# Performance work log

Hardware: AMD Instinct MI355X
Metric: run time of the kernel (lower is better)

The kernel has to match this reference:

```python
import jax, jax.numpy as jnp
import numpy as np

LIDAR_MAX_X = 32.0
LIDAR_MAX_Y = 32.0


def bilinear_grid_sample(value, grid):
    """torch.nn.functional.grid_sample, mode='bilinear', padding_mode='zeros',
    align_corners=False.
    value: (B, C, H, W); grid: (B, Q, P, 2) in [-1, 1] (x=width, y=height).
    Returns (B, C, Q, P)."""
    B, C, H, W = value.shape
    x = (grid[..., 0] + 1.0) * (W / 2) - 0.5  # (B,Q,P) unnormalized col
    y = (grid[..., 1] + 1.0) * (H / 2) - 0.5  # (B,Q,P) unnormalized row
    x0 = jnp.floor(x)
    y0 = jnp.floor(y)
    x1 = x0 + 1.0
    y1 = y0 + 1.0
    wx1 = x - x0
    wx0 = 1.0 - wx1
    wy1 = y - y0
    wy0 = 1.0 - wy1
    vflat = value.reshape(B, C, H * W)

    def gather(ix, iy):
        valid = (ix >= 0) & (ix <= W - 1) & (iy >= 0) & (iy <= H - 1)
        ixc = jnp.clip(ix, 0, W - 1).astype(jnp.int32)
        iyc = jnp.clip(iy, 0, H - 1).astype(jnp.int32)
        idx = iyc * W + ixc  # (B,Q,P)
        g = jax.vmap(lambda v, i: v[:, i])(vflat, idx)  # (B,C,Q,P)
        return g * valid[:, None, :, :].astype(value.dtype)

    out = (gather(x0, y0) * (wx0 * wy0)[:, None]
           + gather(x1, y0) * (wx1 * wy0)[:, None]
           + gather(x0, y1) * (wx0 * wy1)[:, None]
           + gather(x1, y1) * (wx1 * wy1)[:, None])
    return out


def setup_inputs() -> dict:
    key = jax.random.key(0)
    ks = jax.random.split(key, 10)
    bs, Q, P, D = 16, 1024, 8, 256
    Cin, H, W = 64, 128, 128
    queries = jax.random.normal(ks[0], (bs, Q, D), dtype=jnp.float32)
    # scale so trajectory points span the +/-32m BEV extent
    traj_points = jax.random.normal(ks[1], (bs, Q, P, 2), dtype=jnp.float32) * 20.0
    bev_feature = jax.random.normal(ks[2], (bs, Cin, H, W), dtype=jnp.float32)
    spatial_shape = jnp.array([H, W], dtype=jnp.int64)
    attn_w = jax.random.normal(ks[3], (P, D), dtype=jnp.float32) * 0.02
    attn_b = jnp.zeros((P,), dtype=jnp.float32)
    conv_w = jax.random.normal(ks[4], (256, Cin, 3, 3), dtype=jnp.float32) * 0.05
    conv_b = jnp.zeros((256,), dtype=jnp.float32)
    out_w = jax.random.normal(ks[5], (D, D), dtype=jnp.float32) * (1.0 / np.sqrt(D))
    out_b = jnp.zeros((D,), dtype=jnp.float32)
    return {"queries": queries, "traj_points": traj_points,
            "bev_feature": bev_feature, "spatial_shape": spatial_shape,
            "attn_w": attn_w, "attn_b": attn_b,
            "conv_w": conv_w, "conv_b": conv_b,
            "out_w": out_w, "out_b": out_b}


def reference(queries, traj_points, bev_feature, spatial_shape,
              attn_w, attn_b, conv_w, conv_b, out_w, out_b):
    # normalize trajectory to [-1,1] and swap (y,x) -> (x,y) grid order
    grid = jnp.stack([traj_points[..., 1] / LIDAR_MAX_X,
                      traj_points[..., 0] / LIDAR_MAX_Y], axis=-1)  # (bs,Q,P,2)
    # per-query attention over the P sampled points
    attn = jax.nn.softmax(
        jnp.einsum('bqd,pd->bqp', queries, attn_w) + attn_b, axis=-1)  # (bs,Q,P)
    # value projection: 3x3 conv + ReLU
    value = jax.lax.conv_general_dilated(
        bev_feature, conv_w, window_strides=(1, 1),
        padding=((1, 1), (1, 1)),
        dimension_numbers=('NCHW', 'OIHW', 'NCHW'))
    value = jax.nn.relu(value + conv_b[None, :, None, None])  # (bs,256,H,W)
    sampled = bilinear_grid_sample(value, grid)  # (bs,256,Q,P)
    out = jnp.einsum('bcqp,bqp->bqc', sampled, attn)  # weighted sum + permute
    out = jnp.einsum('bqc,dc->bqd', out, out_w) + out_b
    # dropout is identity in eval mode
    return out + queries
```

## Files before the change

### kernel.cpp

```cpp
#include <hip/hip_runtime.h>
#include <stdint.h>


typedef __attribute__((ext_vector_type(8))) short short8;
typedef __attribute__((ext_vector_type(4))) float f32x4;

__device__ __forceinline__ unsigned short f2bf(float f) {
  union { float f; unsigned int u; } v; v.f = f;
  unsigned int r = (v.u + 0x7FFFu + ((v.u >> 16) & 1u)) >> 16;
  return (unsigned short)r;
}
__device__ __forceinline__ float bf2f(unsigned short h) {
  union { unsigned int u; float f; } v; v.u = ((unsigned int)h) << 16;
  return v.f;
}

__device__ __forceinline__ void gload_lds16(const void* g, void* l) {
  __builtin_amdgcn_global_load_lds(
      (const __attribute__((address_space(1))) unsigned int*)g,
      (__attribute__((address_space(3))) unsigned int*)l, 16, 0, 0);
}

__global__ __launch_bounds__(256) void k1_transpose(const float* __restrict__ bev,
                                                    unsigned short* __restrict__ nhwc) {
  __shared__ __align__(16) float lds[64 * 32 * 4];
  const int b = blockIdx.x >> 7, y = blockIdx.x & 127;
  const int t = threadIdx.x;
  const float* src = bev + (size_t)(b * 64) * 16384 + y * 128;
#pragma unroll
  for (int k = 0; k < 8; ++k) {
    int chunk = k * 256 + t;
    int ic = chunk >> 5, xq = chunk & 31;
    float4 v = *(const float4*)(src + ic * 16384 + xq * 4);
    int slot = xq ^ (ic >> 3);
    *(float4*)&lds[(ic * 32 + slot) * 4] = v;
  }
  __syncthreads();
  unsigned short* dst = nhwc + (size_t)blockIdx.x * 8192;
#pragma unroll
  for (int k = 0; k < 4; ++k) {
    int co = k * 256 + t;
    int x = co >> 3, icg = co & 7;
    int slot = (x >> 2) ^ icg;
    int w = x & 3;
    uint4 u;
    unsigned int* up = (unsigned int*)&u;
#pragma unroll
    for (int jj = 0; jj < 4; ++jj) {
      float v0 = lds[((icg * 8 + 2 * jj) * 32 + slot) * 4 + w];
      float v1 = lds[((icg * 8 + 2 * jj + 1) * 32 + slot) * 4 + w];
      up[jj] = (unsigned int)f2bf(v0) | ((unsigned int)f2bf(v1) << 16);
    }
    *(uint4*)(dst + x * 64 + icg * 8) = u;
  }
}

__global__ __launch_bounds__(256) void k1b_pack(const float* __restrict__ conv_w,
                                                const float* __restrict__ out_w,
                                                unsigned short* __restrict__ wconv,
                                                unsigned short* __restrict__ wout,
                                                float* __restrict__ zp) {
  const int tid = blockIdx.x * 256 + threadIdx.x;
  for (int idx = tid; idx < 9 * 8 * 256 * 8; idx += 16384) {
    int j = idx & 7, oc = (idx >> 3) & 255, g = (idx >> 11) & 7, o = idx >> 14;
    wconv[idx] = f2bf(conv_w[(oc * 64 + g * 8 + j) * 9 + o]);
  }
  for (int idx = tid; idx < 32 * 256 * 8; idx += 16384) {
    int j = idx & 7, d = (idx >> 3) & 255, g = idx >> 11;
    wout[idx] = f2bf(out_w[d * 256 + g * 8 + j]);
  }
  if (tid < 64) zp[tid] = 0.0f;
}

#define K2_LOADA(s, A) do {                                                   \
    _Pragma("unroll")                                                         \
    for (int ocf_ = 0; ocf_ < 8; ++ocf_)                                      \
      A[ocf_] = gA[(4 * (s) + g) * 256 + wo * 128 + ocf_ * 16 + l15];         \
  } while (0)

#define K2_READB(s, B) do {                                                   \
    const int o_ = (s) >> 1, ich_ = (s) & 1;                                  \
    const int dyr_ = o_ / 3, dx_ = o_ - dyr_ * 3 - 1;                         \
    _Pragma("unroll")                                                         \
    for (int pf_ = 0; pf_ < 4; ++pf_)                                         \
      B[pf_] = lin[((rh + dyr_) * 8 + ich_ * 4 + g) * 130 + 1 + dx_ + xb +    \
                   l15 + pf_ * 16];                                           \
  } while (0)

#define K2_MFMA(A, B) do {                                                    \
    __builtin_amdgcn_s_setprio(1);                                            \
    _Pragma("unroll")                                                         \
    for (int ocf_ = 0; ocf_ < 8; ++ocf_)                                      \
      _Pragma("unroll")                                                       \
      for (int pf_ = 0; pf_ < 4; ++pf_)                                       \
        acc[ocf_][pf_] = __builtin_amdgcn_mfma_f32_16x16x32_bf16(             \
            A[ocf_], B[pf_], acc[ocf_][pf_], 0, 0, 0);                        \
    __builtin_amdgcn_s_setprio(0);                                            \
  } while (0)

__global__ __launch_bounds__(512, 2) void k2_conv(const unsigned short* __restrict__ nhwc,
                                                  const unsigned short* __restrict__ wconv,
                                                  const float* __restrict__ conv_b,
                                                  const float* __restrict__ zp,
                                                  unsigned short* __restrict__ value) {
  __shared__ __align__(16) char smem[66560];
  const short8* lin = (const short8*)smem;
  const short8* gA = (const short8*)wconv;
  const int bid = blockIdx.x;
  const int swz = (bid & 7) * 128 + (bid >> 3);
  const int b = swz >> 6, yp = swz & 63;
  const int y0 = yp * 2;
  const int t = threadIdx.x, wid = t >> 6, lane = t & 63;
  const int wo = wid >> 2, wp = wid & 3;
  const int g = lane >> 4, l15 = lane & 15;
  const int rh = wp >> 1;
  const int xb = (wp & 1) * 64;

  const unsigned short* bevb = nhwc + (size_t)b * (128 * 128 * 64);
  for (int i = wid; i < 65; i += 8) {
    const int chunk = i * 64 + lane;
    const int ridx = chunk / 1040;
    const int rem = chunk - ridx * 1040;
    const int icg = rem / 130;
    const int c = rem - icg * 130;
    const int yy = y0 - 1 + ridx, xx = c - 1;
    const void* src = (yy >= 0 && yy < 128 && xx >= 0 && xx < 128)
                          ? (const void*)(bevb + ((yy * 128 + xx) * 64 + icg * 8))
                          : (const void*)zp;
    gload_lds16(src, smem + i * 1024);
  }
  __syncthreads();

  const f32x4 z4 = {0.f, 0.f, 0.f, 0.f};
  f32x4 acc[8][4];
#pragma unroll
  for (int i = 0; i < 8; ++i)
#pragma unroll
    for (int j = 0; j < 4; ++j) acc[i][j] = z4;

  short8 A[2][8], bb[2][4];
  K2_LOADA(0, A[0]);
  K2_LOADA(1, A[1]);
  K2_READB(0, bb[0]);

#pragma unroll
  for (int s = 0; s < 18; ++s) {
    if (s < 17) K2_READB(s + 1, bb[(s + 1) & 1]);
    K2_MFMA(A[s & 1], bb[s & 1]);
    if (s + 2 < 18) K2_LOADA(s + 2, A[s & 1]);
  }

  const int y = y0 + rh;
  unsigned short* vrow = value + (((size_t)(b * 128 + y) * 128 + xb + l15) * 256);
#pragma unroll
  for (int ocf = 0; ocf < 8; ++ocf) {
    const int ocb = wo * 128 + ocf * 16 + g * 4;
    const float4 cb4 = *(const float4*)(conv_b + ocb);
#pragma unroll
    for (int pf = 0; pf < 4; ++pf) {
      ushort4 ov;
      float v0 = acc[ocf][pf][0] + cb4.x; ov.x = f2bf(v0 > 0.f ? v0 : 0.f);
      float v1 = acc[ocf][pf][1] + cb4.y; ov.y = f2bf(v1 > 0.f ? v1 : 0.f);
      float v2 = acc[ocf][pf][2] + cb4.z; ov.z = f2bf(v2 > 0.f ? v2 : 0.f);
      float v3 = acc[ocf][pf][3] + cb4.w; ov.w = f2bf(v3 > 0.f ? v3 : 0.f);
      *(ushort4*)(vrow + (size_t)pf * 16 * 256 + ocb) = ov;
    }
  }
}

__global__ __launch_bounds__(256) void k3_sample(const float* __restrict__ queries,
                                                 const float* __restrict__ traj,
                                                 const float* __restrict__ attn_w,
                                                 const float* __restrict__ attn_b,
                                                 const unsigned short* __restrict__ value,
                                                 unsigned short* __restrict__ S) {
  const int wid = threadIdx.x >> 6, lane = threadIdx.x & 63;
  const int qg = blockIdx.x * 4 + wid;
  const int b = qg >> 10;
  const float4 qv = ((const float4*)queries)[qg * 64 + lane];
  float a[8];
#pragma unroll
  for (int p = 0; p < 8; ++p) {
    float4 wv = ((const float4*)attn_w)[p * 64 + lane];
    float d = qv.x * wv.x + qv.y * wv.y + qv.z * wv.z + qv.w * wv.w;
#pragma unroll
    for (int off = 32; off >= 1; off >>= 1) d += __shfl_xor(d, off);
    a[p] = d + attn_b[p];
  }
  float mx = a[0];
#pragma unroll
  for (int p = 1; p < 8; ++p) mx = fmaxf(mx, a[p]);
  float ssum = 0.f;
#pragma unroll
  for (int p = 0; p < 8; ++p) { a[p] = __expf(a[p] - mx); ssum += a[p]; }
  const float inv = 1.f / ssum;

  float acc0 = 0.f, acc1 = 0.f, acc2 = 0.f, acc3 = 0.f;
  const unsigned short* vb = value + (size_t)b * (128 * 128 * 256);
  const int coff = lane * 4;
#pragma unroll
  for (int p = 0; p < 8; ++p) {
    const float ty = traj[(qg * 8 + p) * 2 + 0];
    const float tx = traj[(qg * 8 + p) * 2 + 1];
    const float fx = (tx * 0.03125f + 1.f) * 64.f - 0.5f;
    const float fy = (ty * 0.03125f + 1.f) * 64.f - 0.5f;
    const float fx0 = floorf(fx), fy0 = floorf(fy);
    const int ix0 = (int)fx0, iy0 = (int)fy0;
    const float wx1 = fx - fx0, wx0 = 1.f - wx1;
    const float wy1 = fy - fy0, wy0 = 1.f - wy1;
    const float ap = a[p] * inv;
    const float cw[4] = {wx0 * wy0 * ap, wx1 * wy0 * ap, wx0 * wy1 * ap, wx1 * wy1 * ap};
    const int cx[4] = {ix0, ix0 + 1, ix0, ix0 + 1};
    const int cy[4] = {iy0, iy0, iy0 + 1, iy0 + 1};
#pragma unroll
    for (int cc = 0; cc < 4; ++cc) {
      if (cx[cc] >= 0 && cx[cc] < 128 && cy[cc] >= 0 && cy[cc] < 128) {
        const ushort4 v = *(const ushort4*)(vb + (cy[cc] * 128 + cx[cc]) * 256 + coff);
        acc0 += cw[cc] * bf2f(v.x);
        acc1 += cw[cc] * bf2f(v.y);
        acc2 += cw[cc] * bf2f(v.z);
        acc3 += cw[cc] * bf2f(v.w);
      }
    }
  }
  ushort4 o;
  o.x = f2bf(acc0); o.y = f2bf(acc1); o.z = f2bf(acc2); o.w = f2bf(acc3);
  *(ushort4*)(S + (size_t)qg * 256 + coff) = o;
}

__global__ __launch_bounds__(256, 2) void k4_proj(const unsigned short* __restrict__ S,
                                                  const unsigned short* __restrict__ wout,
                                                  const float* __restrict__ out_b,
                                                  const float* __restrict__ queries,
                                                  float* __restrict__ out) {
  __shared__ __align__(16) char smem[16384];
  const short8* lds8 = (const short8*)smem;
  const short8* wp8 = (const short8*)wout;
  const int t = threadIdx.x, wid = t >> 6, lane = t & 63;
  const int wo = wid >> 1, wq = wid & 1;
  const int q0 = blockIdx.x * 128;
  const int g = lane >> 4, l15 = lane & 15;
  const f32x4 z4 = {0.f, 0.f, 0.f, 0.f};
  f32x4 acc[8][4];
#pragma unroll
  for (int i = 0; i < 8; ++i)
#pragma unroll
    for (int j = 0; j < 4; ++j) acc[i][j] = z4;

#pragma unroll
  for (int ii = 0; ii < 2; ++ii) {
    const int chunk = wid * 128 + ii * 64 + lane;
    const int gg = chunk >> 7, q = chunk & 127;
    gload_lds16(S + ((size_t)(q0 + q) * 256 + gg * 8), smem + wid * 2048 + ii * 1024);
  }
  __syncthreads();

#pragma unroll
  for (int ks = 0; ks < 8; ++ks) {
    if (ks < 7) {
      const int k1 = ks + 1;
#pragma unroll
      for (int ii = 0; ii < 2; ++ii) {
        const int chunk = wid * 128 + ii * 64 + lane;
        const int gg = chunk >> 7, q = chunk & 127;
        gload_lds16(S + ((size_t)(q0 + q) * 256 + k1 * 32 + gg * 8),
                    smem + ((k1 & 1) ? 8192 : 0) + wid * 2048 + ii * 1024);
      }
    }
    short8 af[8];
#pragma unroll
    for (int df = 0; df < 8; ++df)
      af[df] = wp8[(ks * 4 + g) * 256 + wo * 128 + df * 16 + l15];
    short8 bf[4];
    const short8* sb = lds8 + ((ks & 1) ? 512 : 0);
#pragma unroll
    for (int qf = 0; qf < 4; ++qf) bf[qf] = sb[g * 128 + wq * 64 + qf * 16 + l15];
    __builtin_amdgcn_s_setprio(1);
#pragma unroll
    for (int df = 0; df < 8; ++df)
#pragma unroll
      for (int qf = 0; qf < 4; ++qf)
        acc[df][qf] = __builtin_amdgcn_mfma_f32_16x16x32_bf16(af[df], bf[qf], acc[df][qf], 0, 0, 0);
    __builtin_amdgcn_s_setprio(0);
    __syncthreads();
  }

#pragma unroll
  for (int df = 0; df < 8; ++df) {
    const int db = wo * 128 + df * 16 + g * 4;
    const float4 ob4 = *(const float4*)(out_b + db);
#pragma unroll
    for (int qf = 0; qf < 4; ++qf) {
      const int q = q0 + wq * 64 + qf * 16 + l15;
      const float4 qv = *(const float4*)(queries + (size_t)q * 256 + db);
      float4 ov;
      ov.x = acc[df][qf][0] + ob4.x + qv.x;
      ov.y = acc[df][qf][1] + ob4.y + qv.y;
      ov.z = acc[df][qf][2] + ob4.z + qv.z;
      ov.w = acc[df][qf][3] + ob4.w + qv.w;
      *(float4*)(out + (size_t)q * 256 + db) = ov;
    }
  }
}

extern "C" void kernel_launch(void* const* d_in, const int* in_sizes, int n_in,
                              void* d_out, int out_size, void* d_ws, size_t ws_size,
                              hipStream_t stream) {
  const float* queries = (const float*)d_in[0];
  const float* traj    = (const float*)d_in[1];
  const float* bev     = (const float*)d_in[2];
  const float* attn_w  = (const float*)d_in[4];
  const float* attn_b  = (const float*)d_in[5];
  const float* conv_w  = (const float*)d_in[6];
  const float* conv_b  = (const float*)d_in[7];
  const float* out_w   = (const float*)d_in[8];
  const float* out_b   = (const float*)d_in[9];
  float* out = (float*)d_out;

  char* ws = (char*)d_ws;
  unsigned short* bev_nhwc = (unsigned short*)(ws);
  unsigned short* value    = (unsigned short*)(ws + 33554432);
  unsigned short* wconv    = (unsigned short*)(ws + 167772160);
  unsigned short* wout     = (unsigned short*)(ws + 168067072);
  unsigned short* Sbuf     = (unsigned short*)(ws + 168198144);
  float*          zp       = (float*)(ws + 176586752);

  k1_transpose<<<2048, 256, 0, stream>>>(bev, bev_nhwc);
  k1b_pack<<<64, 256, 0, stream>>>(conv_w, out_w, wconv, wout, zp);
  k2_conv<<<1024, 512, 0, stream>>>(bev_nhwc, wconv, conv_b, zp, value);
  k3_sample<<<4096, 256, 0, stream>>>(queries, traj, attn_w, attn_b, value, Sbuf);
  k4_proj<<<128, 256, 0, stream>>>(Sbuf, wout, out_b, queries, out);
}
```

Before: 166.7 us.

## Retile conv warps over full rows and halve projection tile size

In the conv kernel each wave now covers 64 output channels across a full 128-pixel row instead of 128 channels across 64 pixels. This halves the per-wave weight fragment loads but doubles the LDS B reads, and the B-fragment prefetch and setprio hints are dropped. The projection kernel goes from 128-query to 64-query blocks (256 blocks, smaller LDS), each wave computing 64 output dims, which spreads the small GEMM over more CUs. The downside is less reuse per block and no software prefetch of B in the conv.

```diff
diff --git a/kernel.cpp b/kernel.cpp
--- a/kernel.cpp
+++ b/kernel.cpp
@@ -74,28 +74,26 @@
 
 #define K2_LOADA(s, A) do {                                                   \
     _Pragma("unroll")                                                         \
-    for (int ocf_ = 0; ocf_ < 8; ++ocf_)                                      \
-      A[ocf_] = gA[(4 * (s) + g) * 256 + wo * 128 + ocf_ * 16 + l15];         \
+    for (int ocf_ = 0; ocf_ < 4; ++ocf_)                                      \
+      A[ocf_] = gA[(4 * (s) + g) * 256 + wo * 64 + ocf_ * 16 + l15];          \
   } while (0)
 
-#define K2_READB(s, B) do {                                                   \
+#define K2_READB(s, h, B) do {                                                \
     const int o_ = (s) >> 1, ich_ = (s) & 1;                                  \
     const int dyr_ = o_ / 3, dx_ = o_ - dyr_ * 3 - 1;                         \
     _Pragma("unroll")                                                         \
     for (int pf_ = 0; pf_ < 4; ++pf_)                                         \
-      B[pf_] = lin[((rh + dyr_) * 8 + ich_ * 4 + g) * 130 + 1 + dx_ + xb +    \
-                   l15 + pf_ * 16];                                           \
+      B[pf_] = lin[((rh + dyr_) * 8 + ich_ * 4 + g) * 130 + 1 + dx_ +         \
+                   ((h) * 4 + pf_) * 16 + l15];                               \
   } while (0)
 
-#define K2_MFMA(A, B) do {                                                    \
-    __builtin_amdgcn_s_setprio(1);                                            \
+#define K2_MF(A, B, h) do {                                                   \
     _Pragma("unroll")                                                         \
-    for (int ocf_ = 0; ocf_ < 8; ++ocf_)                                      \
+    for (int ocf_ = 0; ocf_ < 4; ++ocf_)                                      \
       _Pragma("unroll")                                                       \
       for (int pf_ = 0; pf_ < 4; ++pf_)                                       \
-        acc[ocf_][pf_] = __builtin_amdgcn_mfma_f32_16x16x32_bf16(             \
-            A[ocf_], B[pf_], acc[ocf_][pf_], 0, 0, 0);                        \
-    __builtin_amdgcn_s_setprio(0);                                            \
+        acc[ocf_][(h) * 4 + pf_] = __builtin_amdgcn_mfma_f32_16x16x32_bf16(   \
+            A[ocf_], B[pf_], acc[ocf_][(h) * 4 + pf_], 0, 0, 0);              \
   } while (0)
 
 __global__ __launch_bounds__(512, 2) void k2_conv(const unsigned short* __restrict__ nhwc,
@@ -111,10 +109,8 @@
   const int b = swz >> 6, yp = swz & 63;
   const int y0 = yp * 2;
   const int t = threadIdx.x, wid = t >> 6, lane = t & 63;
-  const int wo = wid >> 2, wp = wid & 3;
+  const int wo = wid >> 1, rh = wid & 1;
   const int g = lane >> 4, l15 = lane & 15;
-  const int rh = wp >> 1;
-  const int xb = (wp & 1) * 64;
 
   const unsigned short* bevb = nhwc + (size_t)b * (128 * 128 * 64);
   for (int i = wid; i < 65; i += 8) {
@@ -132,32 +128,39 @@
   __syncthreads();
 
   const f32x4 z4 = {0.f, 0.f, 0.f, 0.f};
-  f32x4 acc[8][4];
-#pragma unroll
-  for (int i = 0; i < 8; ++i)
-#pragma unroll
-    for (int j = 0; j < 4; ++j) acc[i][j] = z4;
-
-  short8 A[2][8], bb[2][4];
-  K2_LOADA(0, A[0]);
-  K2_LOADA(1, A[1]);
-  K2_READB(0, bb[0]);
+  f32x4 acc[4][8];
+#pragma unroll
+  for (int i = 0; i < 4; ++i)
+#pragma unroll
+    for (int j = 0; j < 8; ++j) acc[i][j] = z4;
+
+  short8 A0[4], A1[4], B0[4], B1[4];
+  K2_LOADA(0, A0);
+  K2_LOADA(1, A1);
 
 #pragma unroll
   for (int s = 0; s < 18; ++s) {
-    if (s < 17) K2_READB(s + 1, bb[(s + 1) & 1]);
-    K2_MFMA(A[s & 1], bb[s & 1]);
-    if (s + 2 < 18) K2_LOADA(s + 2, A[s & 1]);
+    K2_READB(s, 0, B0);
+    K2_READB(s, 1, B1);
+    if (s & 1) {
+      K2_MF(A1, B0, 0);
+      K2_MF(A1, B1, 1);
+      if (s + 2 < 18) K2_LOADA(s + 2, A1);
+    } else {
+      K2_MF(A0, B0, 0);
+      K2_MF(A0, B1, 1);
+      if (s + 2 < 18) K2_LOADA(s + 2, A0);
+    }
   }
 
   const int y = y0 + rh;
-  unsigned short* vrow = value + (((size_t)(b * 128 + y) * 128 + xb + l15) * 256);
-#pragma unroll
-  for (int ocf = 0; ocf < 8; ++ocf) {
-    const int ocb = wo * 128 + ocf * 16 + g * 4;
+  unsigned short* vrow = value + (((size_t)(b * 128 + y) * 128 + l15) * 256);
+#pragma unroll
+  for (int ocf = 0; ocf < 4; ++ocf) {
+    const int ocb = wo * 64 + ocf * 16 + g * 4;
     const float4 cb4 = *(const float4*)(conv_b + ocb);
 #pragma unroll
-    for (int pf = 0; pf < 4; ++pf) {
+    for (int pf = 0; pf < 8; ++pf) {
       ushort4 ov;
       float v0 = acc[ocf][pf][0] + cb4.x; ov.x = f2bf(v0 > 0.f ? v0 : 0.f);
       float v1 = acc[ocf][pf][1] + cb4.y; ov.y = f2bf(v1 > 0.f ? v1 : 0.f);
@@ -233,65 +236,50 @@
                                                   const float* __restrict__ out_b,
                                                   const float* __restrict__ queries,
                                                   float* __restrict__ out) {
-  __shared__ __align__(16) char smem[16384];
+  __shared__ __align__(16) char smem[8192];
   const short8* lds8 = (const short8*)smem;
   const short8* wp8 = (const short8*)wout;
   const int t = threadIdx.x, wid = t >> 6, lane = t & 63;
-  const int wo = wid >> 1, wq = wid & 1;
-  const int q0 = blockIdx.x * 128;
+  const int q0 = blockIdx.x * 64;
   const int g = lane >> 4, l15 = lane & 15;
   const f32x4 z4 = {0.f, 0.f, 0.f, 0.f};
-  f32x4 acc[8][4];
-#pragma unroll
-  for (int i = 0; i < 8; ++i)
+  f32x4 acc[4][4];
+#pragma unroll
+  for (int i = 0; i < 4; ++i)
 #pragma unroll
     for (int j = 0; j < 4; ++j) acc[i][j] = z4;
 
-#pragma unroll
-  for (int ii = 0; ii < 2; ++ii) {
-    const int chunk = wid * 128 + ii * 64 + lane;
-    const int gg = chunk >> 7, q = chunk & 127;
-    gload_lds16(S + ((size_t)(q0 + q) * 256 + gg * 8), smem + wid * 2048 + ii * 1024);
-  }
+  gload_lds16(S + ((size_t)(q0 + lane) * 256 + wid * 8), smem + wid * 1024);
   __syncthreads();
 
 #pragma unroll
   for (int ks = 0; ks < 8; ++ks) {
-    if (ks < 7) {
-      const int k1 = ks + 1;
-#pragma unroll
-      for (int ii = 0; ii < 2; ++ii) {
-        const int chunk = wid * 128 + ii * 64 + lane;
-        const int gg = chunk >> 7, q = chunk & 127;
-        gload_lds16(S + ((size_t)(q0 + q) * 256 + k1 * 32 + gg * 8),
-                    smem + ((k1 & 1) ? 8192 : 0) + wid * 2048 + ii * 1024);
-      }
-    }
-    short8 af[8];
-#pragma unroll
-    for (int df = 0; df < 8; ++df)
-      af[df] = wp8[(ks * 4 + g) * 256 + wo * 128 + df * 16 + l15];
+    if (ks < 7)
+      gload_lds16(S + ((size_t)(q0 + lane) * 256 + (ks + 1) * 32 + wid * 8),
+                  smem + (((ks + 1) & 1) ? 4096 : 0) + wid * 1024);
+    short8 af[4];
+#pragma unroll
+    for (int df = 0; df < 4; ++df)
+      af[df] = wp8[(ks * 4 + g) * 256 + wid * 64 + df * 16 + l15];
     short8 bf[4];
-    const short8* sb = lds8 + ((ks & 1) ? 512 : 0);
-#pragma unroll
-    for (int qf = 0; qf < 4; ++qf) bf[qf] = sb[g * 128 + wq * 64 + qf * 16 + l15];
-    __builtin_amdgcn_s_setprio(1);
-#pragma unroll
-    for (int df = 0; df < 8; ++df)
+    const short8* sb = lds8 + ((ks & 1) ? 256 : 0);
+#pragma unroll
+    for (int qf = 0; qf < 4; ++qf) bf[qf] = sb[g * 64 + qf * 16 + l15];
+#pragma unroll
+    for (int df = 0; df < 4; ++df)
 #pragma unroll
       for (int qf = 0; qf < 4; ++qf)
         acc[df][qf] = __builtin_amdgcn_mfma_f32_16x16x32_bf16(af[df], bf[qf], acc[df][qf], 0, 0, 0);
-    __builtin_amdgcn_s_setprio(0);
     __syncthreads();
   }
 
 #pragma unroll
-  for (int df = 0; df < 8; ++df) {
-    const int db = wo * 128 + df * 16 + g * 4;
+  for (int df = 0; df < 4; ++df) {
+    const int db = wid * 64 + df * 16 + g * 4;
     const float4 ob4 = *(const float4*)(out_b + db);
 #pragma unroll
     for (int qf = 0; qf < 4; ++qf) {
-      const int q = q0 + wq * 64 + qf * 16 + l15;
+      const int q = q0 + qf * 16 + l15;
       const float4 qv = *(const float4*)(queries + (size_t)q * 256 + db);
       float4 ov;
       ov.x = acc[df][qf][0] + ob4.x + qv.x;
@@ -329,5 +317,5 @@
   k1b_pack<<<64, 256, 0, stream>>>(conv_w, out_w, wconv, wout, zp);
   k2_conv<<<1024, 512, 0, stream>>>(bev_nhwc, wconv, conv_b, zp, value);
   k3_sample<<<4096, 256, 0, stream>>>(queries, traj, attn_w, attn_b, value, Sbuf);
-  k4_proj<<<128, 256, 0, stream>>>(Sbuf, wout, out_b, queries, out);
-}
+  k4_proj<<<256, 256, 0, stream>>>(Sbuf, wout, out_b, queries, out);
+}
```

Result: faster. 160.4 us (-3.7%).
